# Kernel tuning notes

Measured on AMD Instinct MI355X. Metric: run time of the kernel, lower is better.

The kernel has to match this reference:

```python
import jax, jax.numpy as jnp
import numpy as np


def setup_inputs() -> dict:
    key = jax.random.key(0)
    k1, k2 = jax.random.split(key)
    B, C, H, W = 32, 64, 64, 64
    K = 512
    z_e = jax.random.normal(k1, (B, C, H, W), dtype=jnp.float32)
    # codebook initialized uniform(-1/K, 1/K) as in the torch module
    codebook = jax.random.uniform(k2, (K, C), dtype=jnp.float32,
                                  minval=-1.0 / K, maxval=1.0 / K)
    return {"z_e": z_e, "codebook": codebook}


def reference(z_e, codebook):
    B, C, H, W = z_e.shape
    commitment_cost = 0.25
    # [B*H*W, C]
    z_flat = jnp.transpose(z_e, (0, 2, 3, 1)).reshape(-1, C)
    dists = (jnp.sum(z_flat * z_flat, axis=1, keepdims=True)
             + jnp.sum(codebook * codebook, axis=1)
             - 2.0 * jnp.matmul(z_flat, codebook.T))
    encoding_indices = jnp.argmin(dists, axis=1)  # [N] int
    z_q = codebook[encoding_indices].reshape(B, H, W, C)
    z_q = jnp.transpose(z_q, (0, 3, 1, 2))  # [B, C, H, W]
    q_loss = jnp.mean((z_q - jax.lax.stop_gradient(z_e)) ** 2)
    e_loss = jnp.mean((z_e - jax.lax.stop_gradient(z_q)) ** 2)
    loss = q_loss + commitment_cost * e_loss
    # straight-through estimator
    z_q_st = z_e + jax.lax.stop_gradient(z_q - z_e)
    return (z_q_st, encoding_indices, loss)
```

## Files before the change

### kernel.cpp

```cpp
#include <hip/hip_runtime.h>
#include <cfloat>

typedef __attribute__((ext_vector_type(8))) short short8;
typedef __attribute__((ext_vector_type(4))) float f32x4;

constexpr int C_DIM    = 64;
constexpr int K_CODES  = 512;
constexpr int HW       = 4096;
constexpr int CHW      = 262144;
constexpr int NPTS     = 131072;
constexpr int ZQ_SIZE  = 8388608;
constexpr int IDX_OFF  = ZQ_SIZE;
constexpr int LOSS_OFF = ZQ_SIZE + NPTS;
constexpr int TILE     = 128;
constexpr int CHUNK    = 256;
constexpr int NSLOT    = 16;
constexpr size_t WS_BF16 = (size_t)K_CODES * C_DIM * 2;
constexpr size_t WS_NEED = WS_BF16 + (size_t)K_CODES * 4;

__device__ __forceinline__ unsigned short f32_to_bf16_rne(float f) {
    unsigned u = __float_as_uint(f);
    unsigned r = u + 0x7fffu + ((u >> 16) & 1u);
    return (unsigned short)(r >> 16);
}

template <int STRIDE>
__device__ __forceinline__ float np_sumsq64(const float* __restrict__ a) {
    float r[8];
#pragma unroll
    for (int j = 0; j < 8; ++j) { const float v = a[j * STRIDE]; r[j] = __fmul_rn(v, v); }
#pragma unroll
    for (int i = 8; i < 64; i += 8)
#pragma unroll
        for (int j = 0; j < 8; ++j) {
            const float v = a[(i + j) * STRIDE];
            r[j] = __fadd_rn(r[j], __fmul_rn(v, v));
        }
    return __fadd_rn(
        __fadd_rn(__fadd_rn(r[0], r[1]), __fadd_rn(r[2], r[3])),
        __fadd_rn(__fadd_rn(r[4], r[5]), __fadd_rn(r[6], r[7])));
}

__device__ __forceinline__ float np_sumsq64_half_hw(const float* __restrict__ a, int j0) {
    float r[4];
#pragma unroll
    for (int jj = 0; jj < 4; ++jj) {
        const float v = a[(j0 * 4 + jj) * HW];
        r[jj] = __fmul_rn(v, v);
    }
#pragma unroll
    for (int i = 8; i < 64; i += 8)
#pragma unroll
        for (int jj = 0; jj < 4; ++jj) {
            const float v = a[(i + j0 * 4 + jj) * HW];
            r[jj] = __fadd_rn(r[jj], __fmul_rn(v, v));
        }
    return __fadd_rn(__fadd_rn(r[0], r[1]), __fadd_rn(r[2], r[3]));
}

__global__ void vq_zero(float* __restrict__ out) { out[LOSS_OFF] = 0.0f; }

__global__ void vq_prep(const float* __restrict__ cb, unsigned short* __restrict__ wsb,
                        float* __restrict__ wsB, float* __restrict__ out) {
    const int gid = blockIdx.x * 256 + threadIdx.x;
    wsb[gid] = f32_to_bf16_rne(cb[gid]);
    if (gid < K_CODES) wsB[gid] = np_sumsq64<1>(cb + gid * C_DIM);
    if (gid == 0) out[LOSS_OFF] = 0.0f;
}

__global__ __launch_bounds__(256, 4) void vq_idx(const float* __restrict__ ze,
                                                 const float* __restrict__ cb,
                                                 float* __restrict__ out,
                                                 const unsigned short* __restrict__ wsb,
                                                 const float* __restrict__ wsB,
                                                 int use_ws)
{
    __shared__ unsigned short eh[CHUNK * C_DIM];
    __shared__ float  BsL[K_CODES];
    __shared__ float  As[TILE];
    __shared__ unsigned short cand[TILE * NSLOT];
    __shared__ int    cnt[TILE];
    __shared__ int    bestk[TILE];
    __shared__ double lred[4];

    const int tid  = threadIdx.x;
    const int lane = tid & 63, w = tid >> 6;
    const int quad = lane >> 4, l15 = lane & 15;
    const int n0   = blockIdx.x * TILE;
    const int b    = n0 >> 12, hw0 = n0 & (HW - 1);
    const float* zebase = ze + b * CHW + hw0;

    auto stage = [&](int ch) {
        const int row = tid;
        uint4* base = (uint4*)eh;
        if (use_ws) {
            const uint4* src = (const uint4*)(wsb + (size_t)(ch * CHUNK + row) * C_DIM);
#pragma unroll
            for (int s = 0; s < 8; ++s) base[row * 8 + (s ^ (row & 7))] = src[s];
        } else {
            const float4* src = (const float4*)(cb + (size_t)(ch * CHUNK + row) * C_DIM);
#pragma unroll
            for (int s = 0; s < 8; ++s) {
                const float4 f0 = src[2 * s], f1 = src[2 * s + 1];
                uint4 o;
                o.x = (unsigned)f32_to_bf16_rne(f0.x) | ((unsigned)f32_to_bf16_rne(f0.y) << 16);
                o.y = (unsigned)f32_to_bf16_rne(f0.z) | ((unsigned)f32_to_bf16_rne(f0.w) << 16);
                o.z = (unsigned)f32_to_bf16_rne(f1.x) | ((unsigned)f32_to_bf16_rne(f1.y) << 16);
                o.w = (unsigned)f32_to_bf16_rne(f1.z) | ((unsigned)f32_to_bf16_rne(f1.w) << 16);
                base[row * 8 + (s ^ (row & 7))] = o;
            }
        }
    };

    if (use_ws) { for (int k = tid; k < K_CODES; k += 256) BsL[k] = wsB[k]; }
    else        { for (int k = tid; k < K_CODES; k += 256) BsL[k] = np_sumsq64<1>(cb + k * C_DIM); }
    if (tid < TILE) cnt[tid] = 0;
    stage(0);
    {
        const int ptA = tid >> 1, j0 = tid & 1;
        const float p = np_sumsq64_half_hw(zebase + ptA, j0);
        const float o = __shfl_xor(p, 1, 64);
        if (j0 == 0) As[ptA] = __fadd_rn(p, o);
    }

    short8 afr[2][2];
    float  A_pt[2][4], thr[2][4], runmin[2][4];
#pragma unroll
    for (int rt = 0; rt < 2; ++rt) {
        const int pt = w * 32 + rt * 16 + l15;
#pragma unroll
        for (int kc = 0; kc < 2; ++kc) {
            union { unsigned short s[8]; short8 v; } u;
#pragma unroll
            for (int j = 0; j < 8; ++j) {
                const int c = kc * 32 + quad * 8 + j;
                u.s[j] = f32_to_bf16_rne(zebase[c * HW + pt]);
            }
            afr[rt][kc] = u.v;
        }
#pragma unroll
        for (int r = 0; r < 4; ++r) runmin[rt][r] = FLT_MAX;
    }
    __syncthreads();
#pragma unroll
    for (int rt = 0; rt < 2; ++rt)
#pragma unroll
        for (int r = 0; r < 4; ++r)
            A_pt[rt][r] = As[w * 32 + rt * 16 + quad * 4 + r];

    for (int ch = 0; ch < 2; ++ch) {
        if (ch) { __syncthreads(); stage(ch); __syncthreads(); }
        const uint4* ebase = (const uint4*)eh;
#pragma unroll 4
        for (int tile = 0; tile < 16; ++tile) {
            const int cl = tile * 16 + l15;
            const short8 b0 = *(const short8*)&ebase[cl * 8 + ((quad    ) ^ (cl & 7))];
            const short8 b1 = *(const short8*)&ebase[cl * 8 + ((quad + 4) ^ (cl & 7))];
            const float bs = BsL[ch * CHUNK + cl];
#pragma unroll
            for (int rt = 0; rt < 2; ++rt) {
                f32x4 acc = {0.f, 0.f, 0.f, 0.f};
                acc = __builtin_amdgcn_mfma_f32_16x16x32_bf16(afr[rt][0], b0, acc, 0, 0, 0);
                acc = __builtin_amdgcn_mfma_f32_16x16x32_bf16(afr[rt][1], b1, acc, 0, 0, 0);
#pragma unroll
                for (int r = 0; r < 4; ++r) {
                    const float D = fmaf(-2.f, acc[r], __fadd_rn(A_pt[rt][r], bs));
                    runmin[rt][r] = fminf(runmin[rt][r], D);
                }
            }
        }
    }
#pragma unroll
    for (int rt = 0; rt < 2; ++rt)
#pragma unroll
        for (int r = 0; r < 4; ++r) {
            float v = runmin[rt][r];
#pragma unroll
            for (int m = 1; m < 16; m <<= 1) v = fminf(v, __shfl_xor(v, m, 64));
            thr[rt][r] = v + (4e-4f * sqrtf(A_pt[rt][r]) + 3e-4f);
        }

    auto scan_push = [&](int ch) {
        const uint4* ebase = (const uint4*)eh;
#pragma unroll 4
        for (int tile = 0; tile < 16; ++tile) {
            const int cl = tile * 16 + l15;
            const short8 b0 = *(const short8*)&ebase[cl * 8 + ((quad    ) ^ (cl & 7))];
            const short8 b1 = *(const short8*)&ebase[cl * 8 + ((quad + 4) ^ (cl & 7))];
            const float bs = BsL[ch * CHUNK + cl];
#pragma unroll
            for (int rt = 0; rt < 2; ++rt) {
                f32x4 acc = {0.f, 0.f, 0.f, 0.f};
                acc = __builtin_amdgcn_mfma_f32_16x16x32_bf16(afr[rt][0], b0, acc, 0, 0, 0);
                acc = __builtin_amdgcn_mfma_f32_16x16x32_bf16(afr[rt][1], b1, acc, 0, 0, 0);
#pragma unroll
                for (int r = 0; r < 4; ++r) {
                    const float D = fmaf(-2.f, acc[r], __fadd_rn(A_pt[rt][r], bs));
                    if (D <= thr[rt][r]) {
                        const int pt = w * 32 + rt * 16 + quad * 4 + r;
                        const int p = atomicAdd(&cnt[pt], 1);
                        if (p < NSLOT) cand[pt * NSLOT + p] = (unsigned short)(ch * CHUNK + cl);
                    }
                }
            }
        }
    };
    scan_push(1);
    __syncthreads(); stage(0); __syncthreads();
    scan_push(0);
    __syncthreads();

    {
        const int pt = tid >> 1, j0 = tid & 1;
        const int c = cnt[pt];
        if (c <= NSLOT) {
            const float Av = As[pt];
            float bD = FLT_MAX; int bK = K_CODES;
            for (int i = j0; i < c; i += 2) {
                const int k = cand[pt * NSLOT + i];
                const float* er = cb + k * C_DIM;
                float M = 0.f;
#pragma unroll
                for (int cc = 0; cc < 64; ++cc) M = fmaf(zebase[cc * HW + pt], er[cc], M);
                const float D = fmaf(-2.f, M, __fadd_rn(Av, BsL[k]));
                if (D < bD || (D == bD && k < bK)) { bD = D; bK = k; }
            }
            const float oD = __shfl_xor(bD, 1, 64);
            const int   oK = __shfl_xor(bK, 1, 64);
            if (oD < bD || (oD == bD && oK < bK)) { bD = oD; bK = oK; }
            if (j0 == 0) { bestk[pt] = bK; out[IDX_OFF + n0 + pt] = (float)bK; }
        }
    }
    __syncthreads();

    for (int pp = 0; pp < 32; ++pp) {
        const int pt = w * 32 + pp;
        if (cnt[pt] <= NSLOT) continue;
        const float Av = As[pt];
        float bD = FLT_MAX; int bK = K_CODES;
        for (int k = lane; k < K_CODES; k += 64) {
            const float* er = cb + k * C_DIM;
            float M = 0.f;
#pragma unroll
            for (int cc = 0; cc < 64; ++cc) M = fmaf(zebase[cc * HW + pt], er[cc], M);
            const float D = fmaf(-2.f, M, __fadd_rn(Av, BsL[k]));
            if (D < bD || (D == bD && k < bK)) { bD = D; bK = k; }
        }
#pragma unroll
        for (int off = 1; off < 64; off <<= 1) {
            const float oD = __shfl_xor(bD, off, 64);
            const int   oK = __shfl_xor(bK, off, 64);
            if (oD < bD || (oD == bD && oK < bK)) { bD = oD; bK = oK; }
        }
        if (lane == 0) { bestk[pt] = bK; out[IDX_OFF + n0 + pt] = (float)bK; }
    }
    __syncthreads();

    double ls = 0.0;
#pragma unroll
    for (int it = 0; it < 8; ++it) {
        const int task = tid + 256 * it;
        const int c = task >> 5, q = task & 31;
        const float4 xz = *(const float4*)(zebase + c * HW + 4 * q);
        float o[4];
#pragma unroll
        for (int j = 0; j < 4; ++j) {
            const int k = bestk[4 * q + j];
            const float ev = cb[k * C_DIM + c];
            const float xv = (j == 0) ? xz.x : (j == 1) ? xz.y : (j == 2) ? xz.z : xz.w;
            const float d = __fsub_rn(ev, xv);
            o[j] = __fadd_rn(xv, d);
            ls = fma((double)d, (double)d, ls);
        }
        *(float4*)(out + b * CHW + c * HW + hw0 + 4 * q) = make_float4(o[0], o[1], o[2], o[3]);
    }
#pragma unroll
    for (int off = 32; off > 0; off >>= 1) ls += __shfl_xor(ls, off, 64);
    if ((tid & 63) == 0) lred[w] = ls;
    __syncthreads();
    if (tid == 0)
        atomicAdd(out + LOSS_OFF,
                  (float)((lred[0] + lred[1] + lred[2] + lred[3]) * (1.25 / (double)ZQ_SIZE)));
}

extern "C" void kernel_launch(void* const* d_in, const int* in_sizes, int n_in,
                              void* d_out, int out_size, void* d_ws, size_t ws_size,
                              hipStream_t stream) {
    (void)in_sizes; (void)n_in; (void)out_size;
    const float* ze = (const float*)d_in[0];
    const float* cb = (const float*)d_in[1];
    float* out = (float*)d_out;
    const int use_ws = (ws_size >= WS_NEED) ? 1 : 0;
    unsigned short* wsb = (unsigned short*)d_ws;
    float* wsB = (float*)((char*)d_ws + WS_BF16);

    if (use_ws) vq_prep<<<(K_CODES * C_DIM) / 256, 256, 0, stream>>>(cb, wsb, wsB, out);
    else        vq_zero<<<1, 1, 0, stream>>>(out);
    vq_idx<<<NPTS / TILE, 256, 0, stream>>>(ze, cb, out, wsb, wsB, use_ws);
}
```

Baseline: 137.5 us.

## Replace second MFMA scan pass with per-lane top-2 tracking and class rescoring

The two-pass approach (min pass, then a threshold re-scan that pushes candidates) is replaced by a single pass that keeps a per-lane best index and second-best distance. Lanes whose second-best is within the threshold push a marker that makes the refinement step rescore all 32 codes of that lane's column class in fp32. This removes the second MFMA sweep and one codebook restage, at the cost of extra registers, select instructions, and possibly heavier fp32 rescoring for ambiguous points. The distance is rescaled (0.5*bs - dot) and the threshold constants are halved to match.

```diff
diff --git a/kernel.cpp b/kernel.cpp
--- a/kernel.cpp
+++ b/kernel.cpp
@@ -124,7 +124,7 @@
     }
 
     short8 afr[2][2];
-    float  A_pt[2][4], thr[2][4], runmin[2][4];
+    float  A_pt[2][4];
 #pragma unroll
     for (int rt = 0; rt < 2; ++rt) {
         const int pt = w * 32 + rt * 16 + l15;
@@ -138,9 +138,17 @@
             }
             afr[rt][kc] = u.v;
         }
-#pragma unroll
-        for (int r = 0; r < 4; ++r) runmin[rt][r] = FLT_MAX;
-    }
+    }
+
+    float d1[2][4], d2[2][4];
+    int   k1[2][4];
+#pragma unroll
+    for (int rt = 0; rt < 2; ++rt)
+#pragma unroll
+        for (int r = 0; r < 4; ++r) {
+            d1[rt][r] = FLT_MAX; d2[rt][r] = FLT_MAX; k1[rt][r] = K_CODES;
+        }
+
     __syncthreads();
 #pragma unroll
     for (int rt = 0; rt < 2; ++rt)
@@ -149,14 +157,15 @@
             A_pt[rt][r] = As[w * 32 + rt * 16 + quad * 4 + r];
 
     for (int ch = 0; ch < 2; ++ch) {
-        if (ch) { __syncthreads(); stage(ch); __syncthreads(); }
+        if (ch) { __syncthreads(); stage(1); __syncthreads(); }
         const uint4* ebase = (const uint4*)eh;
 #pragma unroll 4
         for (int tile = 0; tile < 16; ++tile) {
             const int cl = tile * 16 + l15;
             const short8 b0 = *(const short8*)&ebase[cl * 8 + ((quad    ) ^ (cl & 7))];
             const short8 b1 = *(const short8*)&ebase[cl * 8 + ((quad + 4) ^ (cl & 7))];
-            const float bs = BsL[ch * CHUNK + cl];
+            const int kk = ch * CHUNK + cl;
+            const float bs = BsL[kk];
 #pragma unroll
             for (int rt = 0; rt < 2; ++rt) {
                 f32x4 acc = {0.f, 0.f, 0.f, 0.f};
@@ -164,50 +173,35 @@
                 acc = __builtin_amdgcn_mfma_f32_16x16x32_bf16(afr[rt][1], b1, acc, 0, 0, 0);
 #pragma unroll
                 for (int r = 0; r < 4; ++r) {
-                    const float D = fmaf(-2.f, acc[r], __fadd_rn(A_pt[rt][r], bs));
-                    runmin[rt][r] = fminf(runmin[rt][r], D);
+                    const float s = fmaf(0.5f, bs, -acc[r]);
+                    const float d1o = d1[rt][r];
+                    const bool  c1  = s < d1o;
+                    d2[rt][r] = c1 ? d1o : fminf(s, d2[rt][r]);
+                    k1[rt][r] = c1 ? kk  : k1[rt][r];
+                    d1[rt][r] = c1 ? s   : d1o;
                 }
             }
         }
     }
+
 #pragma unroll
     for (int rt = 0; rt < 2; ++rt)
 #pragma unroll
         for (int r = 0; r < 4; ++r) {
-            float v = runmin[rt][r];
+            float v = d1[rt][r];
 #pragma unroll
             for (int m = 1; m < 16; m <<= 1) v = fminf(v, __shfl_xor(v, m, 64));
-            thr[rt][r] = v + (4e-4f * sqrtf(A_pt[rt][r]) + 3e-4f);
-        }
-
-    auto scan_push = [&](int ch) {
-        const uint4* ebase = (const uint4*)eh;
-#pragma unroll 4
-        for (int tile = 0; tile < 16; ++tile) {
-            const int cl = tile * 16 + l15;
-            const short8 b0 = *(const short8*)&ebase[cl * 8 + ((quad    ) ^ (cl & 7))];
-            const short8 b1 = *(const short8*)&ebase[cl * 8 + ((quad + 4) ^ (cl & 7))];
-            const float bs = BsL[ch * CHUNK + cl];
-#pragma unroll
-            for (int rt = 0; rt < 2; ++rt) {
-                f32x4 acc = {0.f, 0.f, 0.f, 0.f};
-                acc = __builtin_amdgcn_mfma_f32_16x16x32_bf16(afr[rt][0], b0, acc, 0, 0, 0);
-                acc = __builtin_amdgcn_mfma_f32_16x16x32_bf16(afr[rt][1], b1, acc, 0, 0, 0);
-#pragma unroll
-                for (int r = 0; r < 4; ++r) {
-                    const float D = fmaf(-2.f, acc[r], __fadd_rn(A_pt[rt][r], bs));
-                    if (D <= thr[rt][r]) {
-                        const int pt = w * 32 + rt * 16 + quad * 4 + r;
-                        const int p = atomicAdd(&cnt[pt], 1);
-                        if (p < NSLOT) cand[pt * NSLOT + p] = (unsigned short)(ch * CHUNK + cl);
-                    }
-                }
-            }
-        }
-    };
-    scan_push(1);
-    __syncthreads(); stage(0); __syncthreads();
-    scan_push(0);
+            const int pt = w * 32 + rt * 16 + quad * 4 + r;
+            const float thr = v + (2e-4f * sqrtf(A_pt[rt][r]) + 1.5e-4f);
+            if (d1[rt][r] <= thr) {
+                const int p = atomicAdd(&cnt[pt], 1);
+                if (p < NSLOT) cand[pt * NSLOT + p] = (unsigned short)k1[rt][r];
+            }
+            if (d2[rt][r] <= thr) {
+                const int p = atomicAdd(&cnt[pt], 1);
+                if (p < NSLOT) cand[pt * NSLOT + p] = (unsigned short)(0x8000u | (unsigned)l15);
+            }
+        }
     __syncthreads();
 
     {
@@ -216,14 +210,24 @@
         if (c <= NSLOT) {
             const float Av = As[pt];
             float bD = FLT_MAX; int bK = K_CODES;
-            for (int i = j0; i < c; i += 2) {
-                const int k = cand[pt * NSLOT + i];
+            auto score = [&](int k) {
                 const float* er = cb + k * C_DIM;
                 float M = 0.f;
 #pragma unroll
                 for (int cc = 0; cc < 64; ++cc) M = fmaf(zebase[cc * HW + pt], er[cc], M);
                 const float D = fmaf(-2.f, M, __fadd_rn(Av, BsL[k]));
                 if (D < bD || (D == bD && k < bK)) { bD = D; bK = k; }
+            };
+            int par = 0;
+            for (int i = 0; i < c; ++i) {
+                const unsigned e = cand[pt * NSLOT + i];
+                if (e & 0x8000u) {
+                    const int cls = (int)(e & 15u);
+                    for (int m = j0; m < 32; m += 2) score(cls + 16 * m);
+                } else {
+                    if (par == j0) score((int)e);
+                    par ^= 1;
+                }
             }
             const float oD = __shfl_xor(bD, 1, 64);
             const int   oK = __shfl_xor(bK, 1, 64);
```

New measurement: 462.9 us. 237% more time.
